# Kernel tuning notes

Measured on AMD Instinct MI355X. Metric: run time of the kernel, lower is better.

The kernel has to match this reference:

```python
import jax, jax.numpy as jnp
import numpy as np

V = 32000; D = 256; H = 8; L = 2; FF = 1024; S = 512; B = 32
M = 4096          # mem_max_entries
NC = 10           # num_classes
K = 4             # retrieve top-k
TH = 0.5          # write threshold
EPS = 1e-8


def setup_inputs() -> dict:
    key = jax.random.key(0)
    ks = jax.random.split(key, 24)
    s = 0.02
    def nrm(k, shape):
        return jax.random.normal(k, shape, jnp.float32) * s
    return {
        "input_ids": jax.random.randint(ks[0], (B, S), 0, V),
        "tok_emb": nrm(ks[1], (V, D)),
        "pos_emb": nrm(ks[2], (S, D)),
        # per-layer params stacked on leading dim L
        "Wqkv": nrm(ks[3], (L, 3 * D, D)), "bqkv": jnp.zeros((L, 3 * D)),
        "Wo": nrm(ks[4], (L, D, D)), "bo": jnp.zeros((L, D)),
        "ln1_g": jnp.ones((L, D)), "ln1_b": jnp.zeros((L, D)),
        "W1": nrm(ks[5], (L, FF, D)), "b1": jnp.zeros((L, FF)),
        "W2": nrm(ks[6], (L, D, FF)), "b2": jnp.zeros((L, D)),
        "ln2_g": jnp.ones((L, D)), "ln2_b": jnp.zeros((L, D)),
        # write gate MLP (d -> d -> 1, sigmoid)
        "Wg1": nrm(ks[7], (D, D)), "bg1": jnp.zeros((D,)),
        "Wg2": nrm(ks[8], (1, D)), "bg2": jnp.zeros((1,)),
        # classifier
        "Wc": nrm(ks[9], (NC, D)), "bc": jnp.zeros((NC,)),
    }


def _layer_norm(x, g, b):
    m = x.mean(-1, keepdims=True)
    v = ((x - m) ** 2).mean(-1, keepdims=True)
    return (x - m) / jnp.sqrt(v + 1e-5) * g + b


def _encoder_layer(x, Wqkv, bqkv, Wo, bo, g1, b1, W1, bf1, W2, bf2, g2, b2):
    # post-LN TransformerEncoderLayer, relu activation, batch_first
    Bx, Sx, Dx = x.shape
    dh = Dx // H
    qkv = x @ Wqkv.T + bqkv                     # [B,S,3D]
    q, k, v = jnp.split(qkv, 3, axis=-1)
    def heads(t):
        return t.reshape(Bx, Sx, H, dh).transpose(0, 2, 1, 3)  # [B,H,S,dh]
    q, k, v = heads(q), heads(k), heads(v)
    scores = jnp.einsum("bhqd,bhkd->bhqk", q, k) / jnp.sqrt(jnp.float32(dh))
    attn = jax.nn.softmax(scores, axis=-1)
    o = jnp.einsum("bhqk,bhkd->bhqd", attn, v)
    o = o.transpose(0, 2, 1, 3).reshape(Bx, Sx, Dx)
    o = o @ Wo.T + bo
    x = _layer_norm(x + o, g1, b1)
    ff = jax.nn.relu(x @ W1.T + bf1) @ W2.T + bf2
    return _layer_norm(x + ff, g2, b2)


def reference(input_ids, tok_emb, pos_emb, Wqkv, bqkv, Wo, bo, ln1_g, ln1_b,
              W1, b1, W2, b2, ln2_g, ln2_b, Wg1, bg1, Wg2, bg2, Wc, bc):
    Bx, Sx = input_ids.shape
    x = tok_emb[input_ids] + pos_emb[jnp.arange(Sx)][None, :, :]
    for l in range(L):
        x = _encoder_layer(x, Wqkv[l], bqkv[l], Wo[l], bo[l], ln1_g[l], ln1_b[l],
                           W1[l], b1[l], W2[l], b2[l], ln2_g[l], ln2_b[l])
    h = x                                        # [B,S,D]
    cls_state = h[:, 0, :]                       # [B,D]

    # --- write gate: per-token store into external memory (capped FIFO scatter) ---
    flat_h = h.reshape(-1, D)                    # [B*S, D]
    probs = jax.nn.sigmoid(jax.nn.relu(flat_h @ Wg1.T + bg1) @ Wg2.T + bg2)[:, 0]
    mask = probs > TH                            # [B*S]
    slot = jnp.cumsum(mask.astype(jnp.int32)) - 1
    valid = mask & (slot < M)
    idx = jnp.where(valid, slot, M)              # overflow -> dummy row M
    mem = jnp.zeros((M + 1, D), jnp.float32).at[idx].set(flat_h)[:M]
    count = jnp.minimum(mask.sum(), M)
    occupied = jnp.arange(M) < count             # [M]

    # --- top-k cosine retrieval with CLS as query ---
    qn = cls_state / (jnp.linalg.norm(cls_state, axis=-1, keepdims=True) + EPS)
    kn = mem / (jnp.linalg.norm(mem, axis=-1, keepdims=True) + EPS)
    sims = qn @ kn.T                             # [B,M]
    sims = jnp.where(occupied[None, :], sims, -1e9)
    top_sims, top_idx = jax.lax.top_k(sims, K)   # [B,K]
    vals = mem[top_idx]                          # [B,K,D] (unoccupied rows are zero)
    attn = jax.nn.softmax(top_sims, axis=-1)
    mem_vec = jnp.einsum("bk,bkd->bd", attn, vals)
    mem_vec = jnp.where(count > 0, mem_vec, 0.0)

    cls_aug = cls_state + mem_vec
    return cls_aug @ Wc.T + bc                   # [B,NC]
```

## Files before the change

kernel.cpp:

```cpp
#include <hip/hip_runtime.h>
#include <math.h>

#define D_   256
#define H_   8
#define L_   2
#define FF_  1024
#define S_   512
#define B_   32
#define M_   4096
#define NC_  10
#define ROWS (B_*S_)

typedef __attribute__((ext_vector_type(8))) short bf16x8;
typedef __attribute__((ext_vector_type(4))) float f32x4;

__device__ __forceinline__ float wave_sum(float v) {
#pragma unroll
  for (int off = 1; off < 64; off <<= 1) v += __shfl_xor(v, off, 64);
  return v;
}

__device__ __forceinline__ unsigned short bf16_rne(float x) {
  unsigned int b = __float_as_uint(x);
  return (unsigned short)((b + 0x7FFFu + ((b >> 16) & 1u)) >> 16);
}
__device__ __forceinline__ float bf16_f(unsigned short h) {
  return __uint_as_float(((unsigned int)h) << 16);
}
__device__ __forceinline__ unsigned int cvt_pk_bf16(float a, float b) {
  unsigned int r;
  asm volatile("v_cvt_pk_bf16_f32 %0, %1, %2" : "=v"(r) : "v"(a), "v"(b));
  return r;
}

__device__ __forceinline__ void cvt_store(unsigned short* Hq, unsigned short* Lq,
                                          int off, float4 v) {
  float f[4] = {v.x, v.y, v.z, v.w};
  unsigned short h[4], l[4];
#pragma unroll
  for (int i = 0; i < 4; i++) {
    h[i] = bf16_rne(f[i]);
    l[i] = bf16_rne(f[i] - bf16_f(h[i]));
  }
  uint2 hp, lp;
  hp.x = (unsigned int)h[0] | ((unsigned int)h[1] << 16);
  hp.y = (unsigned int)h[2] | ((unsigned int)h[3] << 16);
  lp.x = (unsigned int)l[0] | ((unsigned int)l[1] << 16);
  lp.y = (unsigned int)l[2] | ((unsigned int)l[3] << 16);
  *(uint2*)&Hq[off] = hp;
  *(uint2*)&Lq[off] = lp;
}

__global__ __launch_bounds__(256) void emb_kernel(const int* __restrict__ ids,
                                                  const float* __restrict__ tok,
                                                  const float* __restrict__ pos,
                                                  float* __restrict__ x) {
  const int row  = blockIdx.x * 4 + (threadIdx.x >> 6);
  const int lane = threadIdx.x & 63;
  const int id = ids[row];
  const int s  = row & (S_ - 1);
  const float4 t = *(const float4*)(tok + (size_t)id * D_ + lane * 4);
  const float4 p = *(const float4*)(pos + (size_t)s  * D_ + lane * 4);
  float4 r; r.x = t.x + p.x; r.y = t.y + p.y; r.z = t.z + p.z; r.w = t.w + p.w;
  *(float4*)(x + (size_t)row * D_ + lane * 4) = r;
}

#define LPITCH 40
template<int BM, int RELU>
__global__ __launch_bounds__(512, 4) void gemm_mfma(const float* __restrict__ A,
                                                    const float* __restrict__ Bm,
                                                    const float* __restrict__ bias,
                                                    float* __restrict__ C,
                                                    int M, int N, int K) {
  constexpr int WGM = BM / 64;
  constexpr int WGN = 8 / WGM;
  constexpr int WN  = 128 / WGN;
  constexpr int FN  = WN / 16;
  __shared__ unsigned short Ah[BM * LPITCH];
  __shared__ unsigned short Al[BM * LPITCH];
  __shared__ unsigned short Bh[128 * LPITCH];
  __shared__ unsigned short Bl[128 * LPITCH];

  const int tid  = threadIdx.x;
  const int lane = tid & 63;
  const int wid  = tid >> 6;
  const int wm = wid / WGN, wn = wid % WGN;
  const int m0 = blockIdx.y * BM, n0 = blockIdx.x * 128;
  const int lrow  = lane & 15;
  const int khalf = (lane >> 4) * 8;

  f32x4 acc[4][FN];
#pragma unroll
  for (int i = 0; i < 4; i++)
#pragma unroll
    for (int j = 0; j < FN; j++) acc[i][j] = (f32x4){0.f, 0.f, 0.f, 0.f};

  const float* Abase = A + (size_t)m0 * K;
  const float* Bbase = Bm + (size_t)n0 * K;

  for (int k0 = 0; k0 < K; k0 += 32) {
    __syncthreads();
#pragma unroll
    for (int j = 0; j < BM / 64; j++) {
      const int idx = tid + j * 512;
      const int row = idx >> 3, kq = (idx & 7) << 2;
      const float4 v = *(const float4*)(Abase + (size_t)row * K + k0 + kq);
      cvt_store(Ah, Al, row * LPITCH + kq, v);
    }
#pragma unroll
    for (int j = 0; j < 2; j++) {
      const int idx = tid + j * 512;
      const int row = idx >> 3, kq = (idx & 7) << 2;
      const float4 v = *(const float4*)(Bbase + (size_t)row * K + k0 + kq);
      cvt_store(Bh, Bl, row * LPITCH + kq, v);
    }
    __syncthreads();

    bf16x8 ah[4], al[4], bh[FN], bl[FN];
#pragma unroll
    for (int fm = 0; fm < 4; fm++) {
      const int r = (wm * 64 + fm * 16 + lrow) * LPITCH + khalf;
      ah[fm] = *(const bf16x8*)&Ah[r];
      al[fm] = *(const bf16x8*)&Al[r];
    }
#pragma unroll
    for (int fn = 0; fn < FN; fn++) {
      const int r = (wn * WN + fn * 16 + lrow) * LPITCH + khalf;
      bh[fn] = *(const bf16x8*)&Bh[r];
      bl[fn] = *(const bf16x8*)&Bl[r];
    }
#pragma unroll
    for (int fm = 0; fm < 4; fm++)
#pragma unroll
      for (int fn = 0; fn < FN; fn++) {
        acc[fm][fn] = __builtin_amdgcn_mfma_f32_16x16x32_bf16(ah[fm], bh[fn], acc[fm][fn], 0, 0, 0);
        acc[fm][fn] = __builtin_amdgcn_mfma_f32_16x16x32_bf16(ah[fm], bl[fn], acc[fm][fn], 0, 0, 0);
        acc[fm][fn] = __builtin_amdgcn_mfma_f32_16x16x32_bf16(al[fm], bh[fn], acc[fm][fn], 0, 0, 0);
      }
  }

#pragma unroll
  for (int fm = 0; fm < 4; fm++)
#pragma unroll
    for (int fn = 0; fn < FN; fn++) {
      const int mrow = m0 + wm * 64 + fm * 16 + (lane >> 4) * 4;
      const int ncol = n0 + wn * WN + fn * 16 + (lane & 15);
      const float bi = bias[ncol];
#pragma unroll
      for (int r = 0; r < 4; r++) {
        float v = acc[fm][fn][r] + bi;
        if (RELU) v = fmaxf(v, 0.f);
        C[(size_t)(mrow + r) * N + ncol] = v;
      }
    }
}

#define KPITCH 40
#define VPITCH 520
__global__ __launch_bounds__(512, 2) void attn_mfma(const float* __restrict__ qkv,
                                                    float* __restrict__ o) {
  __shared__ unsigned short Kh[512 * KPITCH];
  __shared__ unsigned short Kl[512 * KPITCH];
  __shared__ unsigned short Vth[32 * VPITCH];
  __shared__ unsigned short Vtl[32 * VPITCH];

  const int bh = blockIdx.x;
  const int b = bh >> 3, h = bh & 7;
  const int tid = threadIdx.x;
  const int lane = tid & 63;
  const int wv = tid >> 6;
  const float* base = qkv + (size_t)b * (S_ * 768) + h * 32;

  if (tid < 256) {
    float v0[32], v1[32];
    const float* p0 = base + (size_t)(2 * tid) * 768 + 512;
    const float* p1 = p0 + 768;
#pragma unroll
    for (int i = 0; i < 8; i++) {
      *(float4*)&v0[i * 4] = *(const float4*)(p0 + i * 4);
      *(float4*)&v1[i * 4] = *(const float4*)(p1 + i * 4);
    }
#pragma unroll
    for (int d = 0; d < 32; d++) {
      const unsigned short h0 = bf16_rne(v0[d]), h1 = bf16_rne(v1[d]);
      const unsigned short l0 = bf16_rne(v0[d] - bf16_f(h0));
      const unsigned short l1 = bf16_rne(v1[d] - bf16_f(h1));
      *(unsigned int*)&Vth[d * VPITCH + 2 * tid] = (unsigned int)h0 | ((unsigned int)h1 << 16);
      *(unsigned int*)&Vtl[d * VPITCH + 2 * tid] = (unsigned int)l0 | ((unsigned int)l1 << 16);
    }
  } else {
    const int t = tid - 256;
#pragma unroll
    for (int rr = 0; rr < 2; rr++) {
      const int k = 2 * t + rr;
      const float* p = base + (size_t)k * 768 + 256;
      float kv[32];
#pragma unroll
      for (int i = 0; i < 8; i++) *(float4*)&kv[i * 4] = *(const float4*)(p + i * 4);
#pragma unroll
      for (int d = 0; d < 32; d += 2) {
        const unsigned short h0 = bf16_rne(kv[d]), h1 = bf16_rne(kv[d + 1]);
        const unsigned short l0 = bf16_rne(kv[d] - bf16_f(h0));
        const unsigned short l1 = bf16_rne(kv[d + 1] - bf16_f(h1));
        *(unsigned int*)&Kh[k * KPITCH + d] = (unsigned int)h0 | ((unsigned int)h1 << 16);
        *(unsigned int*)&Kl[k * KPITCH + d] = (unsigned int)l0 | ((unsigned int)l1 << 16);
      }
    }
  }

  const int q0 = wv * 64;
  bf16x8 qh[4], ql[4];
#pragma unroll
  for (int f = 0; f < 4; f++) {
    const float* qp = base + (size_t)(q0 + f * 16 + (lane & 15)) * 768 + ((lane >> 4) * 8);
    float qq[8];
    *(float4*)&qq[0] = *(const float4*)qp;
    *(float4*)&qq[4] = *(const float4*)(qp + 4);
    bf16x8 vh, vl;
#pragma unroll
    for (int j = 0; j < 8; j++) {
      const float sv = qq[j] * 0.17677669529663687f;
      const unsigned short hh = bf16_rne(sv);
      vh[j] = (short)hh;
      vl[j] = (short)bf16_rne(sv - bf16_f(hh));
    }
    qh[f] = vh; ql[f] = vl;
  }

  __syncthreads();

  f32x4 oacc[2][4];
#pragma unroll
  for (int i = 0; i < 2; i++)
#pragma unroll
    for (int j = 0; j < 4; j++) oacc[i][j] = (f32x4){0.f, 0.f, 0.f, 0.f};
  float lacc[4] = {0.f, 0.f, 0.f, 0.f};

  const int idx01 = (lane & 15) + ((lane & 16) << 1);
  const int idx23 = idx01 + 16;
  const bool hiSel = (lane & 32) != 0;

  for (int kt = 0; kt < S_; kt += 32) {
    bf16x8 kah[2], kal[2];
#pragma unroll
    for (int u = 0; u < 2; u++) {
      const int off = (kt + u * 16 + (lane & 15)) * KPITCH + ((lane >> 4) * 8);
      kah[u] = *(const bf16x8*)&Kh[off];
      kal[u] = *(const bf16x8*)&Kl[off];
    }
    bf16x8 vah[2], val[2];
#pragma unroll
    for (int df = 0; df < 2; df++) {
      const int off = (df * 16 + (lane & 15)) * VPITCH + kt + ((lane >> 4) * 8);
      vah[df] = *(const bf16x8*)&Vth[off];
      val[df] = *(const bf16x8*)&Vtl[off];
    }
    f32x4 s[2][4];
#pragma unroll
    for (int u = 0; u < 2; u++)
#pragma unroll
      for (int f = 0; f < 4; f++) {
        f32x4 a = (f32x4){0.f, 0.f, 0.f, 0.f};
        a = __builtin_amdgcn_mfma_f32_16x16x32_bf16(kal[u], qh[f], a, 0, 0, 0);
        a = __builtin_amdgcn_mfma_f32_16x16x32_bf16(kah[u], ql[f], a, 0, 0, 0);
        a = __builtin_amdgcn_mfma_f32_16x16x32_bf16(kah[u], qh[f], a, 0, 0, 0);
        s[u][f] = a;
      }
    unsigned int ah[2][4][2], alw[2][4][2];
#pragma unroll
    for (int u = 0; u < 2; u++)
#pragma unroll
      for (int f = 0; f < 4; f++) {
        const float p0 = __expf(s[u][f][0]);
        const float p1 = __expf(s[u][f][1]);
        const float p2 = __expf(s[u][f][2]);
        const float p3 = __expf(s[u][f][3]);
        lacc[f] += (p0 + p1) + (p2 + p3);
        const unsigned int h01 = cvt_pk_bf16(p0, p1);
        const unsigned int h23 = cvt_pk_bf16(p2, p3);
        const float r0 = p0 - __uint_as_float(h01 << 16);
        const float r1 = p1 - __uint_as_float(h01 & 0xffff0000u);
        const float r2 = p2 - __uint_as_float(h23 << 16);
        const float r3 = p3 - __uint_as_float(h23 & 0xffff0000u);
        ah[u][f][0] = h01; ah[u][f][1] = h23;
        alw[u][f][0] = cvt_pk_bf16(r0, r1);
        alw[u][f][1] = cvt_pk_bf16(r2, r3);
      }
#pragma unroll
    for (int f = 0; f < 4; f++) {
      union { unsigned int w[4]; bf16x8 v; } ph, pl;
      {
        const unsigned int t0 = (unsigned int)__shfl((int)ah[0][f][0], idx01, 64);
        const unsigned int t1 = (unsigned int)__shfl((int)ah[1][f][0], idx01, 64);
        ph.w[0] = hiSel ? t1 : t0;
      }
      {
        const unsigned int t0 = (unsigned int)__shfl((int)ah[0][f][1], idx01, 64);
        const unsigned int t1 = (unsigned int)__shfl((int)ah[1][f][1], idx01, 64);
        ph.w[1] = hiSel ? t1 : t0;
      }
      {
        const unsigned int t0 = (unsigned int)__shfl((int)ah[0][f][0], idx23, 64);
        const unsigned int t1 = (unsigned int)__shfl((int)ah[1][f][0], idx23, 64);
        ph.w[2] = hiSel ? t1 : t0;
      }
      {
        const unsigned int t0 = (unsigned int)__shfl((int)ah[0][f][1], idx23, 64);
        const unsigned int t1 = (unsigned int)__shfl((int)ah[1][f][1], idx23, 64);
        ph.w[3] = hiSel ? t1 : t0;
      }
      {
        const unsigned int t0 = (unsigned int)__shfl((int)alw[0][f][0], idx01, 64);
        const unsigned int t1 = (unsigned int)__shfl((int)alw[1][f][0], idx01, 64);
        pl.w[0] = hiSel ? t1 : t0;
      }
      {
        const unsigned int t0 = (unsigned int)__shfl((int)alw[0][f][1], idx01, 64);
        const unsigned int t1 = (unsigned int)__shfl((int)alw[1][f][1], idx01, 64);
        pl.w[1] = hiSel ? t1 : t0;
      }
      {
        const unsigned int t0 = (unsigned int)__shfl((int)alw[0][f][0], idx23, 64);
        const unsigned int t1 = (unsigned int)__shfl((int)alw[1][f][0], idx23, 64);
        pl.w[2] = hiSel ? t1 : t0;
      }
      {
        const unsigned int t0 = (unsigned int)__shfl((int)alw[0][f][1], idx23, 64);
        const unsigned int t1 = (unsigned int)__shfl((int)alw[1][f][1], idx23, 64);
        pl.w[3] = hiSel ? t1 : t0;
      }
#pragma unroll
      for (int df = 0; df < 2; df++) {
        oacc[df][f] = __builtin_amdgcn_mfma_f32_16x16x32_bf16(val[df], ph.v, oacc[df][f], 0, 0, 0);
        oacc[df][f] = __builtin_amdgcn_mfma_f32_16x16x32_bf16(vah[df], pl.v, oacc[df][f], 0, 0, 0);
        oacc[df][f] = __builtin_amdgcn_mfma_f32_16x16x32_bf16(vah[df], ph.v, oacc[df][f], 0, 0, 0);
      }
    }
  }

#pragma unroll
  for (int f = 0; f < 4; f++) {
    lacc[f] += __shfl_xor(lacc[f], 16, 64);
    lacc[f] += __shfl_xor(lacc[f], 32, 64);
  }
#pragma unroll
  for (int f = 0; f < 4; f++) {
    const float inv = 1.f / lacc[f];
    const int q = q0 + f * 16 + (lane & 15);
    float* op = o + (size_t)(b * S_ + q) * D_ + h * 32;
#pragma unroll
    for (int df = 0; df < 2; df++) {
      const int dbase = df * 16 + (lane >> 4) * 4;
#pragma unroll
      for (int r = 0; r < 4; r++)
        op[dbase + r] = oacc[df][f][r] * inv;
    }
  }
}

__global__ __launch_bounds__(256) void add_ln(const float* __restrict__ x,
                                              const float* __restrict__ y,
                                              const float* __restrict__ g,
                                              const float* __restrict__ bta,
                                              float* __restrict__ out) {
  const int row  = blockIdx.x * 4 + (threadIdx.x >> 6);
  const int lane = threadIdx.x & 63;
  const size_t base = (size_t)row * D_ + lane * 4;
  const float4 xv = *(const float4*)(x + base);
  const float4 yv = *(const float4*)(y + base);
  float v[4] = {xv.x + yv.x, xv.y + yv.y, xv.z + yv.z, xv.w + yv.w};
  float s = v[0] + v[1] + v[2] + v[3];
  s = wave_sum(s);
  const float mean = s * (1.f / 256.f);
  float d[4] = {v[0] - mean, v[1] - mean, v[2] - mean, v[3] - mean};
  float sq = d[0] * d[0] + d[1] * d[1] + d[2] * d[2] + d[3] * d[3];
  sq = wave_sum(sq);
  const float inv = 1.f / sqrtf(sq * (1.f / 256.f) + 1e-5f);
  const float4 gv = *(const float4*)(g + lane * 4);
  const float4 bv = *(const float4*)(bta + lane * 4);
  float4 r;
  r.x = d[0] * inv * gv.x + bv.x; r.y = d[1] * inv * gv.y + bv.y;
  r.z = d[2] * inv * gv.z + bv.z; r.w = d[3] * inv * gv.w + bv.w;
  *(float4*)(out + base) = r;
}

__global__ __launch_bounds__(256) void gate_mask(const float* __restrict__ t,
                                                 const float* __restrict__ Wg2,
                                                 const float* __restrict__ bg2,
                                                 int* __restrict__ mask) {
  const int row  = blockIdx.x * 4 + (threadIdx.x >> 6);
  const int lane = threadIdx.x & 63;
  const float4 tv = *(const float4*)(t + (size_t)row * D_ + lane * 4);
  const float4 wv = *(const float4*)(Wg2 + lane * 4);
  float s = tv.x * wv.x + tv.y * wv.y + tv.z * wv.z + tv.w * wv.w;
  s = wave_sum(s);
  if (lane == 0) mask[row] = (s + bg2[0]) > 0.f ? 1 : 0;
}

__global__ __launch_bounds__(256) void scan_kernel(const int* __restrict__ mask,
                                                   int* __restrict__ slots,
                                                   int* __restrict__ countp) {
  __shared__ int wtot[4];
  const int tid = threadIdx.x;
  const int lane = tid & 63, wid = tid >> 6;
  const int base = tid * 64;
  int s = 0;
#pragma unroll 8
  for (int i = 0; i < 64; i++) s += mask[base + i];
  int inc = s;
#pragma unroll
  for (int off = 1; off < 64; off <<= 1) {
    const int t = __shfl_up(inc, off, 64);
    if (lane >= off) inc += t;
  }
  if (lane == 63) wtot[wid] = inc;
  __syncthreads();
  int woff = 0;
#pragma unroll
  for (int w = 0; w < 4; w++) woff += (w < wid) ? wtot[w] : 0;
  const int total = wtot[0] + wtot[1] + wtot[2] + wtot[3];
  if (tid == 0) countp[0] = total < M_ ? total : M_;
  int run = woff + inc - s;
  for (int i = 0; i < 64; i++) {
    const int r = base + i;
    const int mk = mask[r];
    slots[r] = (mk && run < M_) ? run : -1;
    run += mk;
  }
}

__global__ __launch_bounds__(256) void scatter_kernel(const float* __restrict__ h,
                                                      const int* __restrict__ slots,
                                                      float* __restrict__ mem) {
  const int row  = blockIdx.x * 4 + (threadIdx.x >> 6);
  const int lane = threadIdx.x & 63;
  const int sl = slots[row];
  if (sl >= 0)
    *(float4*)(mem + (size_t)sl * D_ + lane * 4) =
        *(const float4*)(h + (size_t)row * D_ + lane * 4);
}

__global__ __launch_bounds__(256) void qnorm_kernel(const float* __restrict__ h,
                                                    float* __restrict__ qden) {
  const int b    = blockIdx.x * 4 + (threadIdx.x >> 6);
  const int lane = threadIdx.x & 63;
  const float4 c = *(const float4*)(h + (size_t)b * S_ * D_ + lane * 4);
  float sq = c.x * c.x + c.y * c.y + c.z * c.z + c.w * c.w;
  sq = wave_sum(sq);
  if (lane == 0) qden[b] = sqrtf(sq) + 1e-8f;
}

__global__ __launch_bounds__(256) void sims_kernel(const float* __restrict__ h,
                                                   const float* __restrict__ mem,
                                                   const float* __restrict__ qden,
                                                   const int* __restrict__ countp,
                                                   float* __restrict__ sims) {
  __shared__ float cls[B_ * D_];
  __shared__ float qd[B_];
  const int tid = threadIdx.x;
  const int lane = tid & 63, wid = tid >> 6;
  for (int i = tid; i < B_ * D_ / 4; i += 256) {
    const int flat = i * 4;
    const int b = flat >> 8, d = flat & 255;
    *(float4*)&cls[flat] = *(const float4*)(h + (size_t)b * S_ * D_ + d);
  }
  if (tid < B_) qd[tid] = qden[tid];
  __syncthreads();
  const int count = countp[0];
  const int r = blockIdx.x * 4 + wid;
  const float4 m4 = *(const float4*)(mem + (size_t)r * D_ + lane * 4);
  float sq = m4.x * m4.x + m4.y * m4.y + m4.z * m4.z + m4.w * m4.w;
  sq = wave_sum(sq);
  const float rn = sqrtf(sq) + 1e-8f;
  if (r < count) {
    for (int b = 0; b < B_; b++) {
      const float4 c4 = *(const float4*)&cls[b * D_ + lane * 4];
      float dt = m4.x * c4.x + m4.y * c4.y + m4.z * c4.z + m4.w * c4.w;
      dt = wave_sum(dt);
      if (lane == 0) sims[b * M_ + r] = dt / (qd[b] * rn);
    }
  } else if (lane == 0) {
    for (int b = 0; b < B_; b++) sims[b * M_ + r] = -1e9f;
  }
}

__global__ __launch_bounds__(256) void topk_mix(const float* __restrict__ h,
                                                const float* __restrict__ mem,
                                                const float* __restrict__ simsg,
                                                const int* __restrict__ countp,
                                                const float* __restrict__ Wc,
                                                const float* __restrict__ bc,
                                                float* __restrict__ out) {
  __shared__ float sims[M_];
  __shared__ float cls[D_];
  __shared__ float wv4[4];
  __shared__ int   wi4[4];
  __shared__ float aug[D_];
  __shared__ float tv[4];
  __shared__ int   tix[4];

  const int b = blockIdx.x, tid = threadIdx.x;
  const int lane = tid & 63, wid = tid >> 6;
  const int count = countp[0];

  for (int i = tid; i < M_; i += 256) sims[i] = simsg[b * M_ + i];
  cls[tid] = h[(size_t)b * S_ * D_ + tid];
  __syncthreads();

  for (int k = 0; k < 4; k++) {
    float bv = -INFINITY; int bi = 1 << 30;
#pragma unroll
    for (int rr = 0; rr < M_ / 256; rr++) {
      const int r = tid + rr * 256;
      const float v = sims[r];
      if (v > bv || (v == bv && r < bi)) { bv = v; bi = r; }
    }
#pragma unroll
    for (int off = 1; off < 64; off <<= 1) {
      const float ov = __shfl_xor(bv, off, 64);
      const int   oi = __shfl_xor(bi, off, 64);
      if (ov > bv || (ov == bv && oi < bi)) { bv = ov; bi = oi; }
    }
    if (lane == 0) { wv4[wid] = bv; wi4[wid] = bi; }
    __syncthreads();
    if (tid == 0) {
      float bb = wv4[0]; int bbi = wi4[0];
#pragma unroll
      for (int i = 1; i < 4; i++)
        if (wv4[i] > bb || (wv4[i] == bb && wi4[i] < bbi)) { bb = wv4[i]; bbi = wi4[i]; }
      tv[k] = bb; tix[k] = bbi; sims[bbi] = -INFINITY;
    }
    __syncthreads();
  }

  float w[4];
  {
    const float mx = tv[0];
    float ws = 0.f;
#pragma unroll
    for (int k = 0; k < 4; k++) { w[k] = expf(tv[k] - mx); ws += w[k]; }
    const float inv = 1.f / ws;
#pragma unroll
    for (int k = 0; k < 4; k++) w[k] *= inv;
  }

  {
    float mv = 0.f;
    if (count > 0) {
#pragma unroll
      for (int k = 0; k < 4; k++) mv = fmaf(w[k], mem[(size_t)tix[k] * D_ + tid], mv);
    }
    aug[tid] = cls[tid] + mv;
  }
  __syncthreads();

  const float4 a4 = *(const float4*)&aug[lane * 4];
  for (int c = wid; c < NC_; c += 4) {
    const float4 wc = *(const float4*)(Wc + (size_t)c * D_ + lane * 4);
    float dt = a4.x * wc.x + a4.y * wc.y + a4.z * wc.z + a4.w * wc.w;
    dt = wave_sum(dt);
    if (lane == 0) out[b * NC_ + c] = dt + bc[c];
  }
}

extern "C" void kernel_launch(void* const* d_in, const int* in_sizes, int n_in,
                              void* d_out, int out_size, void* d_ws, size_t ws_size,
                              hipStream_t stream) {
  const int*   ids  = (const int*)d_in[0];
  const float* tok  = (const float*)d_in[1];
  const float* pos  = (const float*)d_in[2];
  const float* Wqkv = (const float*)d_in[3];
  const float* bqkv = (const float*)d_in[4];
  const float* Wo   = (const float*)d_in[5];
  const float* bo   = (const float*)d_in[6];
  const float* ln1g = (const float*)d_in[7];
  const float* ln1b = (const float*)d_in[8];
  const float* W1   = (const float*)d_in[9];
  const float* b1   = (const float*)d_in[10];
  const float* W2   = (const float*)d_in[11];
  const float* b2   = (const float*)d_in[12];
  const float* ln2g = (const float*)d_in[13];
  const float* ln2b = (const float*)d_in[14];
  const float* Wg1  = (const float*)d_in[15];
  const float* bg1  = (const float*)d_in[16];
  const float* Wg2  = (const float*)d_in[17];
  const float* bg2  = (const float*)d_in[18];
  const float* Wc   = (const float*)d_in[19];
  const float* bc   = (const float*)d_in[20];
  float* out = (float*)d_out;

  float* xA   = (float*)d_ws;
  float* xB   = xA  + (size_t)ROWS * D_;
  float* ob   = xB  + (size_t)ROWS * D_;
  float* pb   = ob  + (size_t)ROWS * D_;
  float* big  = pb  + (size_t)ROWS * D_;
  float* mem  = big + (size_t)ROWS * FF_;
  float* qden = mem + (size_t)M_ * D_;
  float* sims = qden + 64;
  int*   mask = (int*)(sims + (size_t)B_ * M_);
  int*   slots = mask + ROWS;
  int*   cnt   = slots + ROWS;

  emb_kernel<<<ROWS / 4, 256, 0, stream>>>(ids, tok, pos, xA);

  for (int l = 0; l < L_; l++) {
    gemm_mfma<128, 0><<<dim3(768 / 128, ROWS / 128), 512, 0, stream>>>(
        xA, Wqkv + (size_t)l * 768 * 256, bqkv + l * 768, big, ROWS, 768, 256);
    attn_mfma<<<B_ * H_, 512, 0, stream>>>(big, ob);
    gemm_mfma<64, 0><<<dim3(256 / 128, ROWS / 64), 512, 0, stream>>>(
        ob, Wo + (size_t)l * 256 * 256, bo + l * 256, pb, ROWS, 256, 256);
    add_ln<<<ROWS / 4, 256, 0, stream>>>(xA, pb, ln1g + l * 256, ln1b + l * 256, xB);
    gemm_mfma<128, 1><<<dim3(1024 / 128, ROWS / 128), 512, 0, stream>>>(
        xB, W1 + (size_t)l * 1024 * 256, b1 + l * 1024, big, ROWS, 1024, 256);
    gemm_mfma<64, 0><<<dim3(256 / 128, ROWS / 64), 512, 0, stream>>>(
        big, W2 + (size_t)l * 256 * 1024, b2 + l * 256, pb, ROWS, 256, 1024);
    add_ln<<<ROWS / 4, 256, 0, stream>>>(xB, pb, ln2g + l * 256, ln2b + l * 256, xA);
  }

  gemm_mfma<64, 1><<<dim3(256 / 128, ROWS / 64), 512, 0, stream>>>(
      xA, Wg1, bg1, ob, ROWS, 256, 256);
  gate_mask<<<ROWS / 4, 256, 0, stream>>>(ob, Wg2, bg2, mask);
  scan_kernel<<<1, 256, 0, stream>>>(mask, slots, cnt);
  (void)hipMemsetAsync(mem, 0, (size_t)M_ * D_ * sizeof(float), stream);
  scatter_kernel<<<ROWS / 4, 256, 0, stream>>>(xA, slots, mem);

  qnorm_kernel<<<B_ / 4, 256, 0, stream>>>(xA, qden);
  sims_kernel<<<M_ / 4, 256, 0, stream>>>(xA, mem, qden, cnt, sims);
  topk_mix<<<B_, 256, 0, stream>>>(xA, mem, sims, cnt, Wc, bc, out);
}
```

Baseline: 507.8 us.

## Prefetch GEMM tiles into registers, repad LDS, and restructure attention with permuted K layout

The GEMM now loads the next K-slice from global memory into registers before converting and storing the current slice, which overlaps global latency with MFMA work. LDS pitch shrinks to 36 with 8-byte fragment loads to change the bank-conflict pattern. Attention moves to 1024 threads with 32 queries per wave and splits K and V staging across thread halves. K rows are stored in a permuted order so the P fragments come straight from the score accumulators, which removes the cross-lane shuffles. The costs are extra registers for the prefetch buffers, and a layout that depends on a correct permutation.

```diff
diff --git a/kernel.cpp b/kernel.cpp
--- a/kernel.cpp
+++ b/kernel.cpp
@@ -49,6 +49,13 @@
   lp.y = (unsigned int)l[2] | ((unsigned int)l[3] << 16);
   *(uint2*)&Hq[off] = hp;
   *(uint2*)&Lq[off] = lp;
+}
+
+__device__ __forceinline__ bf16x8 ld_frag(const unsigned short* p, int off) {
+  union { uint2 u[2]; bf16x8 v; } x;
+  x.u[0] = *(const uint2*)(p + off);
+  x.u[1] = *(const uint2*)(p + off + 4);
+  return x.v;
 }
 
 __global__ __launch_bounds__(256) void emb_kernel(const int* __restrict__ ids,
@@ -65,7 +72,7 @@
   *(float4*)(x + (size_t)row * D_ + lane * 4) = r;
 }
 
-#define LPITCH 40
+#define LP 36
 template<int BM, int RELU>
 __global__ __launch_bounds__(512, 4) void gemm_mfma(const float* __restrict__ A,
                                                     const float* __restrict__ Bm,
@@ -76,10 +83,10 @@
   constexpr int WGN = 8 / WGM;
   constexpr int WN  = 128 / WGN;
   constexpr int FN  = WN / 16;
-  __shared__ unsigned short Ah[BM * LPITCH];
-  __shared__ unsigned short Al[BM * LPITCH];
-  __shared__ unsigned short Bh[128 * LPITCH];
-  __shared__ unsigned short Bl[128 * LPITCH];
+  __shared__ __align__(16) unsigned short Ah[BM * LP];
+  __shared__ __align__(16) unsigned short Al[BM * LP];
+  __shared__ __align__(16) unsigned short Bh[128 * LP];
+  __shared__ __align__(16) unsigned short Bl[128 * LP];
 
   const int tid  = threadIdx.x;
   const int lane = tid & 63;
@@ -89,45 +96,52 @@
   const int lrow  = lane & 15;
   const int khalf = (lane >> 4) * 8;
 
+  const int srow = tid >> 3;
+  const int kq   = (tid & 7) << 2;
+  const float* Aptr = A + (size_t)(m0 + srow) * K + kq;
+  const float* Bptr = Bm + (size_t)(n0 + srow) * K + kq;
+
   f32x4 acc[4][FN];
 #pragma unroll
   for (int i = 0; i < 4; i++)
 #pragma unroll
     for (int j = 0; j < FN; j++) acc[i][j] = (f32x4){0.f, 0.f, 0.f, 0.f};
 
-  const float* Abase = A + (size_t)m0 * K;
-  const float* Bbase = Bm + (size_t)n0 * K;
+  float4 pa[BM / 64], pb[2];
+#pragma unroll
+  for (int j = 0; j < BM / 64; j++) pa[j] = *(const float4*)(Aptr + (size_t)j * 64 * K);
+#pragma unroll
+  for (int j = 0; j < 2; j++) pb[j] = *(const float4*)(Bptr + (size_t)j * 64 * K);
 
   for (int k0 = 0; k0 < K; k0 += 32) {
+    const int kn = (k0 + 32 < K) ? (k0 + 32) : k0;
+    float4 na[BM / 64], nb[2];
+#pragma unroll
+    for (int j = 0; j < BM / 64; j++) na[j] = *(const float4*)(Aptr + (size_t)j * 64 * K + kn);
+#pragma unroll
+    for (int j = 0; j < 2; j++) nb[j] = *(const float4*)(Bptr + (size_t)j * 64 * K + kn);
+
     __syncthreads();
 #pragma unroll
-    for (int j = 0; j < BM / 64; j++) {
-      const int idx = tid + j * 512;
-      const int row = idx >> 3, kq = (idx & 7) << 2;
-      const float4 v = *(const float4*)(Abase + (size_t)row * K + k0 + kq);
-      cvt_store(Ah, Al, row * LPITCH + kq, v);
-    }
-#pragma unroll
-    for (int j = 0; j < 2; j++) {
-      const int idx = tid + j * 512;
-      const int row = idx >> 3, kq = (idx & 7) << 2;
-      const float4 v = *(const float4*)(Bbase + (size_t)row * K + k0 + kq);
-      cvt_store(Bh, Bl, row * LPITCH + kq, v);
-    }
+    for (int j = 0; j < BM / 64; j++)
+      cvt_store(Ah, Al, (srow + j * 64) * LP + kq, pa[j]);
+#pragma unroll
+    for (int j = 0; j < 2; j++)
+      cvt_store(Bh, Bl, (srow + j * 64) * LP + kq, pb[j]);
     __syncthreads();
 
     bf16x8 ah[4], al[4], bh[FN], bl[FN];
 #pragma unroll
     for (int fm = 0; fm < 4; fm++) {
-      const int r = (wm * 64 + fm * 16 + lrow) * LPITCH + khalf;
-      ah[fm] = *(const bf16x8*)&Ah[r];
-      al[fm] = *(const bf16x8*)&Al[r];
+      const int r = (wm * 64 + fm * 16 + lrow) * LP + khalf;
+      ah[fm] = ld_frag(Ah, r);
+      al[fm] = ld_frag(Al, r);
     }
 #pragma unroll
     for (int fn = 0; fn < FN; fn++) {
-      const int r = (wn * WN + fn * 16 + lrow) * LPITCH + khalf;
-      bh[fn] = *(const bf16x8*)&Bh[r];
-      bl[fn] = *(const bf16x8*)&Bl[r];
+      const int r = (wn * WN + fn * 16 + lrow) * LP + khalf;
+      bh[fn] = ld_frag(Bh, r);
+      bl[fn] = ld_frag(Bl, r);
     }
 #pragma unroll
     for (int fm = 0; fm < 4; fm++)
@@ -137,6 +151,10 @@
         acc[fm][fn] = __builtin_amdgcn_mfma_f32_16x16x32_bf16(ah[fm], bl[fn], acc[fm][fn], 0, 0, 0);
         acc[fm][fn] = __builtin_amdgcn_mfma_f32_16x16x32_bf16(al[fm], bh[fn], acc[fm][fn], 0, 0, 0);
       }
+#pragma unroll
+    for (int j = 0; j < BM / 64; j++) pa[j] = na[j];
+#pragma unroll
+    for (int j = 0; j < 2; j++) pb[j] = nb[j];
   }
 
 #pragma unroll
@@ -155,14 +173,14 @@
     }
 }
 
-#define KPITCH 40
-#define VPITCH 520
-__global__ __launch_bounds__(512, 2) void attn_mfma(const float* __restrict__ qkv,
-                                                    float* __restrict__ o) {
-  __shared__ unsigned short Kh[512 * KPITCH];
-  __shared__ unsigned short Kl[512 * KPITCH];
-  __shared__ unsigned short Vth[32 * VPITCH];
-  __shared__ unsigned short Vtl[32 * VPITCH];
+#define KP 36
+#define VP 516
+__global__ __launch_bounds__(1024, 4) void attn_mfma(const float* __restrict__ qkv,
+                                                     float* __restrict__ o) {
+  __shared__ __align__(16) unsigned short Kh[512 * KP];
+  __shared__ __align__(16) unsigned short Kl[512 * KP];
+  __shared__ __align__(16) unsigned short Vth[32 * VP];
+  __shared__ __align__(16) unsigned short Vtl[32 * VP];
 
   const int bh = blockIdx.x;
   const int b = bh >> 3, h = bh & 7;
@@ -171,47 +189,42 @@
   const int wv = tid >> 6;
   const float* base = qkv + (size_t)b * (S_ * 768) + h * 32;
 
-  if (tid < 256) {
-    float v0[32], v1[32];
-    const float* p0 = base + (size_t)(2 * tid) * 768 + 512;
+  if (tid < 512) {
+    const int slot = tid;
+    const int s5 = slot & 31;
+    const int orig = (slot & ~31) + 8 * ((s5 >> 2) & 3) + ((s5 >> 4) << 2) + (s5 & 3);
+    const float* p = base + (size_t)orig * 768 + 256;
+#pragma unroll
+    for (int j = 0; j < 8; j++) {
+      const float4 v = *(const float4*)(p + j * 4);
+      cvt_store(Kh, Kl, slot * KP + j * 4, v);
+    }
+  } else {
+    const int u  = tid - 512;
+    const int kp = u & 255;
+    const int dg = (u >> 8) * 16;
+    const float* p0 = base + (size_t)(2 * kp) * 768 + 512 + dg;
     const float* p1 = p0 + 768;
-#pragma unroll
-    for (int i = 0; i < 8; i++) {
+    float v0[16], v1[16];
+#pragma unroll
+    for (int i = 0; i < 4; i++) {
       *(float4*)&v0[i * 4] = *(const float4*)(p0 + i * 4);
       *(float4*)&v1[i * 4] = *(const float4*)(p1 + i * 4);
     }
 #pragma unroll
-    for (int d = 0; d < 32; d++) {
+    for (int d = 0; d < 16; d++) {
       const unsigned short h0 = bf16_rne(v0[d]), h1 = bf16_rne(v1[d]);
       const unsigned short l0 = bf16_rne(v0[d] - bf16_f(h0));
       const unsigned short l1 = bf16_rne(v1[d] - bf16_f(h1));
-      *(unsigned int*)&Vth[d * VPITCH + 2 * tid] = (unsigned int)h0 | ((unsigned int)h1 << 16);
-      *(unsigned int*)&Vtl[d * VPITCH + 2 * tid] = (unsigned int)l0 | ((unsigned int)l1 << 16);
-    }
-  } else {
-    const int t = tid - 256;
-#pragma unroll
-    for (int rr = 0; rr < 2; rr++) {
-      const int k = 2 * t + rr;
-      const float* p = base + (size_t)k * 768 + 256;
-      float kv[32];
-#pragma unroll
-      for (int i = 0; i < 8; i++) *(float4*)&kv[i * 4] = *(const float4*)(p + i * 4);
-#pragma unroll
-      for (int d = 0; d < 32; d += 2) {
-        const unsigned short h0 = bf16_rne(kv[d]), h1 = bf16_rne(kv[d + 1]);
-        const unsigned short l0 = bf16_rne(kv[d] - bf16_f(h0));
-        const unsigned short l1 = bf16_rne(kv[d + 1] - bf16_f(h1));
-        *(unsigned int*)&Kh[k * KPITCH + d] = (unsigned int)h0 | ((unsigned int)h1 << 16);
-        *(unsigned int*)&Kl[k * KPITCH + d] = (unsigned int)l0 | ((unsigned int)l1 << 16);
-      }
-    }
-  }
-
-  const int q0 = wv * 64;
-  bf16x8 qh[4], ql[4];
-#pragma unroll
-  for (int f = 0; f < 4; f++) {
+      *(unsigned int*)&Vth[(dg + d) * VP + 2 * kp] = (unsigned int)h0 | ((unsigned int)h1 << 16);
+      *(unsigned int*)&Vtl[(dg + d) * VP + 2 * kp] = (unsigned int)l0 | ((unsigned int)l1 << 16);
+    }
+  }
+
+  const int q0 = wv * 32;
+  bf16x8 qh[2], ql[2];
+#pragma unroll
+  for (int f = 0; f < 2; f++) {
     const float* qp = base + (size_t)(q0 + f * 16 + (lane & 15)) * 768 + ((lane >> 4) * 8);
     float qq[8];
     *(float4*)&qq[0] = *(const float4*)qp;
@@ -229,48 +242,44 @@
 
   __syncthreads();
 
-  f32x4 oacc[2][4];
+  f32x4 oacc[2][2];
 #pragma unroll
   for (int i = 0; i < 2; i++)
 #pragma unroll
-    for (int j = 0; j < 4; j++) oacc[i][j] = (f32x4){0.f, 0.f, 0.f, 0.f};
-  float lacc[4] = {0.f, 0.f, 0.f, 0.f};
-
-  const int idx01 = (lane & 15) + ((lane & 16) << 1);
-  const int idx23 = idx01 + 16;
-  const bool hiSel = (lane & 32) != 0;
+    for (int j = 0; j < 2; j++) oacc[i][j] = (f32x4){0.f, 0.f, 0.f, 0.f};
+  float lacc[2] = {0.f, 0.f};
 
   for (int kt = 0; kt < S_; kt += 32) {
     bf16x8 kah[2], kal[2];
 #pragma unroll
     for (int u = 0; u < 2; u++) {
-      const int off = (kt + u * 16 + (lane & 15)) * KPITCH + ((lane >> 4) * 8);
-      kah[u] = *(const bf16x8*)&Kh[off];
-      kal[u] = *(const bf16x8*)&Kl[off];
+      const int off = (kt + u * 16 + (lane & 15)) * KP + ((lane >> 4) * 8);
+      kah[u] = ld_frag(Kh, off);
+      kal[u] = ld_frag(Kl, off);
     }
     bf16x8 vah[2], val[2];
 #pragma unroll
     for (int df = 0; df < 2; df++) {
-      const int off = (df * 16 + (lane & 15)) * VPITCH + kt + ((lane >> 4) * 8);
-      vah[df] = *(const bf16x8*)&Vth[off];
-      val[df] = *(const bf16x8*)&Vtl[off];
-    }
-    f32x4 s[2][4];
+      const int off = (df * 16 + (lane & 15)) * VP + kt + ((lane >> 4) * 8);
+      vah[df] = ld_frag(Vth, off);
+      val[df] = ld_frag(Vtl, off);
+    }
+    f32x4 s[2][2];
 #pragma unroll
     for (int u = 0; u < 2; u++)
 #pragma unroll
-      for (int f = 0; f < 4; f++) {
+      for (int f = 0; f < 2; f++) {
         f32x4 a = (f32x4){0.f, 0.f, 0.f, 0.f};
         a = __builtin_amdgcn_mfma_f32_16x16x32_bf16(kal[u], qh[f], a, 0, 0, 0);
         a = __builtin_amdgcn_mfma_f32_16x16x32_bf16(kah[u], ql[f], a, 0, 0, 0);
         a = __builtin_amdgcn_mfma_f32_16x16x32_bf16(kah[u], qh[f], a, 0, 0, 0);
         s[u][f] = a;
       }
-    unsigned int ah[2][4][2], alw[2][4][2];
-#pragma unroll
-    for (int u = 0; u < 2; u++)
-#pragma unroll
-      for (int f = 0; f < 4; f++) {
+#pragma unroll
+    for (int f = 0; f < 2; f++) {
+      union { unsigned int w[4]; bf16x8 v; } ph, pl;
+#pragma unroll
+      for (int u = 0; u < 2; u++) {
         const float p0 = __expf(s[u][f][0]);
         const float p1 = __expf(s[u][f][1]);
         const float p2 = __expf(s[u][f][2]);
@@ -282,52 +291,10 @@
         const float r1 = p1 - __uint_as_float(h01 & 0xffff0000u);
         const float r2 = p2 - __uint_as_float(h23 << 16);
         const float r3 = p3 - __uint_as_float(h23 & 0xffff0000u);
-        ah[u][f][0] = h01; ah[u][f][1] = h23;
-        alw[u][f][0] = cvt_pk_bf16(r0, r1);
-        alw[u][f][1] = cvt_pk_bf16(r2, r3);
-      }
-#pragma unroll
-    for (int f = 0; f < 4; f++) {
-      union { unsigned int w[4]; bf16x8 v; } ph, pl;
-      {
-        const unsigned int t0 = (unsigned int)__shfl((int)ah[0][f][0], idx01, 64);
-        const unsigned int t1 = (unsigned int)__shfl((int)ah[1][f][0], idx01, 64);
-        ph.w[0] = hiSel ? t1 : t0;
-      }
-      {
-        const unsigned int t0 = (unsigned int)__shfl((int)ah[0][f][1], idx01, 64);
-        const unsigned int t1 = (unsigned int)__shfl((int)ah[1][f][1], idx01, 64);
-        ph.w[1] = hiSel ? t1 : t0;
-      }
-      {
-        const unsigned int t0 = (unsigned int)__shfl((int)ah[0][f][0], idx23, 64);
-        const unsigned int t1 = (unsigned int)__shfl((int)ah[1][f][0], idx23, 64);
-        ph.w[2] = hiSel ? t1 : t0;
-      }
-      {
-        const unsigned int t0 = (unsigned int)__shfl((int)ah[0][f][1], idx23, 64);
-        const unsigned int t1 = (unsigned int)__shfl((int)ah[1][f][1], idx23, 64);
-        ph.w[3] = hiSel ? t1 : t0;
-      }
-      {
-        const unsigned int t0 = (unsigned int)__shfl((int)alw[0][f][0], idx01, 64);
-        const unsigned int t1 = (unsigned int)__shfl((int)alw[1][f][0], idx01, 64);
-        pl.w[0] = hiSel ? t1 : t0;
-      }
-      {
-        const unsigned int t0 = (unsigned int)__shfl((int)alw[0][f][1], idx01, 64);
-        const unsigned int t1 = (unsigned int)__shfl((int)alw[1][f][1], idx01, 64);
-        pl.w[1] = hiSel ? t1 : t0;
-      }
-      {
-        const unsigned int t0 = (unsigned int)__shfl((int)alw[0][f][0], idx23, 64);
-        const unsigned int t1 = (unsigned int)__shfl((int)alw[1][f][0], idx23, 64);
-        pl.w[2] = hiSel ? t1 : t0;
-      }
-      {
-        const unsigned int t0 = (unsigned int)__shfl((int)alw[0][f][1], idx23, 64);
-        const unsigned int t1 = (unsigned int)__shfl((int)alw[1][f][1], idx23, 64);
-        pl.w[3] = hiSel ? t1 : t0;
+        ph.w[u * 2 + 0] = h01;
+        ph.w[u * 2 + 1] = h23;
+        pl.w[u * 2 + 0] = cvt_pk_bf16(r0, r1);
+        pl.w[u * 2 + 1] = cvt_pk_bf16(r2, r3);
       }
 #pragma unroll
       for (int df = 0; df < 2; df++) {
@@ -339,12 +306,12 @@
   }
 
 #pragma unroll
-  for (int f = 0; f < 4; f++) {
+  for (int f = 0; f < 2; f++) {
     lacc[f] += __shfl_xor(lacc[f], 16, 64);
     lacc[f] += __shfl_xor(lacc[f], 32, 64);
   }
 #pragma unroll
-  for (int f = 0; f < 4; f++) {
+  for (int f = 0; f < 2; f++) {
     const float inv = 1.f / lacc[f];
     const int q = q0 + f * 16 + (lane & 15);
     float* op = o + (size_t)(b * S_ + q) * D_ + h * 32;
@@ -606,7 +573,7 @@
   for (int l = 0; l < L_; l++) {
     gemm_mfma<128, 0><<<dim3(768 / 128, ROWS / 128), 512, 0, stream>>>(
         xA, Wqkv + (size_t)l * 768 * 256, bqkv + l * 768, big, ROWS, 768, 256);
-    attn_mfma<<<B_ * H_, 512, 0, stream>>>(big, ob);
+    attn_mfma<<<B_ * H_, 1024, 0, stream>>>(big, ob);
     gemm_mfma<64, 0><<<dim3(256 / 128, ROWS / 64), 512, 0, stream>>>(
         ob, Wo + (size_t)l * 256 * 256, bo + l * 256, pb, ROWS, 256, 256);
     add_ln<<<ROWS / 4, 256, 0, stream>>>(xA, pb, ln1g + l * 256, ln1b + l * 256, xB);
```

Result: faster. 471.9 us (-7.1%).
